# Kernel optimization log

Hardware: AMD Instinct MI355X
Metric: run time of the kernel (lower is better)

Reference implementation:

```python
import math
import jax, jax.numpy as jnp
import numpy as np

# ---- static hyperparams (match init_kwargs) ----
B, D, K, NC, F = 16384, 64, 128, 64, 256
TAU_MIN = 0.01
TAU_DENOM_MIN = 0.001
EPS = 0.001  # transport_eps


def setup_inputs() -> dict:
    key = jax.random.key(0)
    ks = jax.random.split(key, 8)
    # latent positions strictly inside the Poincare ball (norm < 0.9)
    z = jax.random.normal(ks[0], (B, D), jnp.float32)
    z = z / (jnp.linalg.norm(z, axis=-1, keepdims=True) + 1e-6)
    z = z * (0.9 * jax.random.uniform(ks[1], (B, 1), jnp.float32))
    features = jax.random.normal(ks[2], (B, F), jnp.float32)
    q_z_w = jax.random.normal(ks[3], (K, D), jnp.float32) * 0.02
    q_z_b = jnp.zeros((K,), jnp.float32)
    q_feat_w = jax.random.normal(ks[4], (K, F), jnp.float32) * 0.02
    q_feat_b = jnp.zeros((K,), jnp.float32)
    q_gamma = jax.random.normal(ks[5], (K, D, D), jnp.float32) * 0.02
    chart_queries = jax.random.normal(ks[6], (NC, K), jnp.float32) * 0.02
    return {"z": z, "features": features, "q_z_w": q_z_w, "q_z_b": q_z_b,
            "q_feat_w": q_feat_w, "q_feat_b": q_feat_b, "q_gamma": q_gamma,
            "chart_queries": chart_queries}


def _hyperbolic_score(z, centers):
    # z: [B, D]; centers: [NC, D] -> scores [B, NC]
    diff = z[:, None, :] - centers[None, :, :]
    dist_sq = (diff ** 2).sum(-1)                       # [B, NC]
    z_sq = (z ** 2).sum(-1, keepdims=True)              # [B, 1]
    c_sq = (centers ** 2).sum(-1)[None, :]              # [1, NC]
    denom = (1.0 - z_sq) * (1.0 - c_sq)
    arg = 1.0 + 2.0 * dist_sq / (denom + EPS)
    dist = jnp.arccosh(jnp.maximum(arg, 1.0 + EPS))
    # metric-aware temperature tau(z)
    tau = math.sqrt(K) * jnp.maximum(1.0 - z_sq[:, 0], TAU_DENOM_MIN) / 2.0
    tau = jnp.maximum(tau, TAU_MIN)                     # [B]
    return -dist / tau[:, None]


def reference(z, features, q_z_w, q_z_b, q_feat_w, q_feat_b, q_gamma, chart_queries):
    # chart centers live in the first D coords of the chart queries
    centers = chart_queries[:, :D]                      # [NC, D]
    scores = _hyperbolic_score(z, centers)              # [B, NC]

    # query: linear(z) + linear(features) + bilinear gamma term
    q = z @ q_z_w.T + q_z_b + features @ q_feat_w.T + q_feat_b   # [B, K]
    q = q + jnp.einsum("bi,bj,kij->bk", z, z, q_gamma)           # gamma contraction

    # O(n) hyperbolic parallel transport: scale queries by 1/lambda(z)
    r2 = jnp.minimum((z ** 2).sum(-1, keepdims=True), 1.0 - EPS)  # [B, 1]
    lam = 2.0 / (1.0 - r2 + EPS)                                  # [B, 1]
    tq = chart_queries[None, :, :] / lam[:, None, :]              # [B, NC, K]

    scores = scores + jnp.einsum("bk,bnk->bn", q, tq) / math.sqrt(K)
    weights = jax.nn.softmax(scores, axis=-1)           # [B, NC] (soft routing)
    k_chart = jnp.argmax(weights, axis=-1)              # [B]
    return weights, k_chart
```

## Files before the change

kernel.cpp:

```cpp
#include <hip/hip_runtime.h>
#include <hip/hip_bf16.h>
#include <cmath>
#include <cstring>

#define B_TOT 16384

typedef unsigned int uint_t;
typedef unsigned short ushort_t;
typedef __attribute__((ext_vector_type(8))) short bf16x8;
typedef __attribute__((ext_vector_type(16))) float f32x16;

#define WS_TAB 0
#define WS_CSQ 1024
#define WS_LIN 4096
#define WS_S   4198400
#define WS_PPK 5246976

__global__ __launch_bounds__(256) void prep_s(const float* __restrict__ g,
                                              const float* __restrict__ cq,
                                              char* __restrict__ ws) {
  __shared__ float gl[128][68];
  __shared__ float cql[16][132];
  float* S = (float*)(ws + WS_S);
  const int ns = blockIdx.x >> 6, J = blockIdx.x & 63, t = threadIdx.x;
  for (int i = t; i < 2048; i += 256) {
    const int k = i >> 4, c4 = (i & 15) * 4;
    *(float4*)&gl[k][c4] = *(const float4*)(g + (size_t)k * 4096 + J * 64 + c4);
  }
  for (int i = t; i < 2048; i += 256) {
    const int n16 = i >> 7, k = i & 127;
    cql[n16][k] = cq[(ns * 16 + n16) * 128 + k];
  }
  __syncthreads();
  const int n16 = t >> 4, c4 = (t & 15) * 4;
  float4 acc = {0.f, 0.f, 0.f, 0.f};
#pragma unroll 8
  for (int k = 0; k < 128; ++k) {
    const float w = cql[n16][k];
    const float4 gv = *(const float4*)&gl[k][c4];
    acc.x = fmaf(w, gv.x, acc.x);
    acc.y = fmaf(w, gv.y, acc.y);
    acc.z = fmaf(w, gv.z, acc.z);
    acc.w = fmaf(w, gv.w, acc.w);
  }
  *(float4*)(S + (size_t)(ns * 16 + n16) * 4096 + J * 64 + c4) = acc;
}

__global__ __launch_bounds__(256) void prep_pack(
    const float* __restrict__ qfw, const float* __restrict__ cq,
    const float* __restrict__ qzw, const float* __restrict__ qzb,
    const float* __restrict__ qfb, char* __restrict__ ws) {
  __shared__ float Sl[4096];
  __shared__ uint_t tabl[192];
  __shared__ float psumf[128][2];
  const int n = blockIdx.x & 63, part = blockIdx.x >> 6, t = threadIdx.x;
  const float* __restrict__ S = (const float*)(ws + WS_S) + (size_t)n * 4096;
  for (int i = t; i < 4096; i += 256) Sl[i] = S[i];
  if (t < 64) {
    const int i = t;
    const int start = (i < 16) ? 4 * i
                     : (i < 32) ? 64 + 3 * (i - 16)
                     : (i < 48) ? 112 + 2 * (i - 32)
                                : 144 + (i - 48);
    const int nst = 4 - (i >> 4);
    for (int u = 0; u < nst; ++u)
      tabl[start + u] = (0u << 16) | ((uint_t)i << 8) | (uint_t)(16 * ((i >> 4) + u));
  } else if (t < 80) tabl[160 + (t - 64)] = (1u << 16) | (uint_t)((t - 64) * 16);
  else if (t < 84)   tabl[176 + (t - 80)] = (2u << 16) | (uint_t)((t - 80) * 16);
  else if (t == 84)  tabl[180] = (3u << 16);
  else if (t < 96)   tabl[181 + (t - 85)] = 0;
  __syncthreads();
  if (part == 0 && n == 0 && t < 192) ((uint_t*)(ws + WS_TAB))[t] = tabl[t];

  const int mt = n >> 5, r = n & 31;
  auto wpack = [&](int s, int jo, float val) {
    const __hip_bfloat16 hb = __float2bfloat16(val);
    const float hf = __bfloat162float(hb);
    const __hip_bfloat16 lb = __float2bfloat16(val - hf);
    ushort_t hu, lu;
    memcpy(&hu, &hb, 2);
    memcpy(&lu, &lb, 2);
    const size_t base =
        (((size_t)s * 4 + mt * 2) * 64 + ((jo >> 3) & 1) * 32 + r) * 16 + (jo & 7) * 2;
    *(ushort_t*)(ws + WS_PPK + base) = hu;
    *(ushort_t*)(ws + WS_PPK + base + 1024) = lu;
  };

  for (int v = part * 640 + t; v < (part + 1) * 640; v += 256) {
    const int s = v >> 4, jo = v & 15;
    const uint_t inf = tabl[s];
    const int i = (inf >> 8) & 255, j0 = inf & 255;
    const int j = j0 + jo;
    const float val =
        (j < i) ? 0.f : ((j > i) ? Sl[i * 64 + j] + Sl[j * 64 + i] : Sl[i * 64 + i]);
    wpack(s, jo, val);
  }
  const float* __restrict__ cqn = cq + n * 128;

  if (part >= 2) {
    const int fl = t & 127, kh = t >> 7;
    const int f = (part - 2) * 128 + fl;
    float a = 0.f;
#pragma unroll 8
    for (int k = 0; k < 64; ++k)
      a = fmaf(qfw[(kh * 64 + k) * 256 + f], cqn[kh * 64 + k], a);
    psumf[fl][kh] = a;
    __syncthreads();
    if (t < 128) {
      const int ff = (part - 2) * 128 + t;
      wpack(160 + (ff >> 4), ff & 15, psumf[t][0] + psumf[t][1]);
    }
  } else if (part == 1) {
    if (t < 64) {
      float a = 0.f;
#pragma unroll 8
      for (int k = 0; k < 128; ++k) a = fmaf(cqn[k], qzw[k * 64 + t], a);
      wpack(176 + (t >> 4), t & 15, a);
    }
    for (int v2 = t; v2 < 176; v2 += 256) wpack(181 + (v2 >> 4), v2 & 15, 0.f);
  } else {
    if (t == 128) {
      float a = 0.f;
      for (int k = 0; k < 128; ++k) a = fmaf(qzb[k] + qfb[k], cqn[k], a);
      wpack(180, 0, a);
    } else if (t > 128 && t < 144) wpack(180, t - 128, 0.f);
    if (t == 144) {
      double a = 0.0;
      for (int d = 0; d < 64; ++d) a = fma((double)cqn[d], (double)cqn[d], a);
      ((double*)(ws + WS_CSQ))[n] = a;
    }
  }
}

__global__ __launch_bounds__(256, 4) void gemm_tail_kernel(
    const float* __restrict__ z, const float* __restrict__ feat,
    const float* __restrict__ cq, char* __restrict__ ws,
    float* __restrict__ out) {
  __shared__ __align__(16) unsigned char smem[46208];
  float (*z_lds)[68] = (float (*)[68])(smem);
  float (*s_lin)[65] = (float (*)[65])(smem + 8704);
  float (*zt)[33] = (float (*)[33])(smem + 17024);
  float (*cqT)[65] = (float (*)[65])(smem + 25472);
  double (*s_exp)[65] = (double (*)[65])(smem + 25472);
  double (*pmax)[9] = (double (*)[9])(smem + 42112);
  int (*parg)[9] = (int (*)[9])(smem + 44416);
  double* rowmax = (double*)(smem + 45568);
  int* rowarg = (int*)(smem + 45824);
  double* rowinv = (double*)(smem + 45952);

  const int t = threadIdx.x, lane = t & 63;
  const int wv = __builtin_amdgcn_readfirstlane(t >> 6);
  const int b0 = blockIdx.x * 32;
  const int h = lane >> 5, c = lane & 31;

  for (int i = t; i < 2048; i += 256) z_lds[i >> 6][i & 63] = z[(size_t)b0 * 64 + i];
  if (t < 128) z_lds[t >> 2][64 + (t & 3)] = 0.f;
  for (int i = t; i < 32 * 65; i += 256) ((float*)s_lin)[i] = 0.f;
  __syncthreads();

  const bf16x8* __restrict__ pp = (const bf16x8*)(ws + WS_PPK);
  const uint_t* __restrict__ tab = (const uint_t*)(ws + WS_TAB);
  f32x16 acc[2] = {};
#pragma unroll 2
  for (int it = 0; it < 46; ++it) {
    const int s = wv + it * 4;
    const uint_t inf = tab[s];
    const int mode = inf >> 16, i_idx = (inf >> 8) & 255, p0 = inf & 255;
    const bf16x8 Ah0 = pp[((size_t)s * 4 + 0) * 64 + lane];
    const bf16x8 Al0 = pp[((size_t)s * 4 + 1) * 64 + lane];
    const bf16x8 Ah1 = pp[((size_t)s * 4 + 2) * 64 + lane];
    const bf16x8 Al1 = pp[((size_t)s * 4 + 3) * 64 + lane];
    const int bl = c;
    float xv[8];
    if (mode == 0) {
      const float zi = z_lds[bl][i_idx];
      const float* __restrict__ zp = &z_lds[bl][p0 + h * 8];
      const float4 a = *(const float4*)zp, b2 = *(const float4*)(zp + 4);
      xv[0] = zi * a.x; xv[1] = zi * a.y; xv[2] = zi * a.z; xv[3] = zi * a.w;
      xv[4] = zi * b2.x; xv[5] = zi * b2.y; xv[6] = zi * b2.z; xv[7] = zi * b2.w;
    } else if (mode == 1) {
      const float* __restrict__ fp = feat + (size_t)(b0 + bl) * 256 + p0 + h * 8;
      const float4 a = *(const float4*)fp, b2 = *(const float4*)(fp + 4);
      xv[0] = a.x; xv[1] = a.y; xv[2] = a.z; xv[3] = a.w;
      xv[4] = b2.x; xv[5] = b2.y; xv[6] = b2.z; xv[7] = b2.w;
    } else if (mode == 2) {
      const float* __restrict__ zp = &z_lds[bl][p0 + h * 8];
      const float4 a = *(const float4*)zp, b2 = *(const float4*)(zp + 4);
      xv[0] = a.x; xv[1] = a.y; xv[2] = a.z; xv[3] = a.w;
      xv[4] = b2.x; xv[5] = b2.y; xv[6] = b2.z; xv[7] = b2.w;
    } else {
      xv[0] = (h == 0) ? 1.f : 0.f;
      xv[1] = xv[2] = xv[3] = xv[4] = xv[5] = xv[6] = xv[7] = 0.f;
    }
    uint_t bhw[4], blw[4];
#pragma unroll
    for (int e2 = 0; e2 < 4; ++e2) {
      const float2 xp = {xv[2 * e2], xv[2 * e2 + 1]};
      const __hip_bfloat162 hb2 = __float22bfloat162_rn(xp);
      uint_t hw;
      memcpy(&hw, &hb2, 4);
      const float h0 = __uint_as_float(hw << 16);
      const float h1 = __uint_as_float(hw & 0xffff0000u);
      const float2 lp = {xp.x - h0, xp.y - h1};
      const __hip_bfloat162 lb2 = __float22bfloat162_rn(lp);
      uint_t lw;
      memcpy(&lw, &lb2, 4);
      bhw[e2] = hw;
      blw[e2] = lw;
    }
    bf16x8 Bh, Bl;
    memcpy(&Bh, bhw, 16);
    memcpy(&Bl, blw, 16);
    acc[0] = __builtin_amdgcn_mfma_f32_32x32x16_bf16(Ah0, Bh, acc[0], 0, 0, 0);
    acc[0] = __builtin_amdgcn_mfma_f32_32x32x16_bf16(Ah0, Bl, acc[0], 0, 0, 0);
    acc[0] = __builtin_amdgcn_mfma_f32_32x32x16_bf16(Al0, Bh, acc[0], 0, 0, 0);
    acc[1] = __builtin_amdgcn_mfma_f32_32x32x16_bf16(Ah1, Bh, acc[1], 0, 0, 0);
    acc[1] = __builtin_amdgcn_mfma_f32_32x32x16_bf16(Ah1, Bl, acc[1], 0, 0, 0);
    acc[1] = __builtin_amdgcn_mfma_f32_32x32x16_bf16(Al1, Bh, acc[1], 0, 0, 0);
  }
#pragma unroll
  for (int mt = 0; mt < 2; ++mt)
#pragma unroll
    for (int r = 0; r < 16; ++r) {
      const int n = mt * 32 + (r & 3) + 8 * (r >> 2) + 4 * h;
      atomicAdd(&s_lin[c][n], acc[mt][r]);
    }

  for (int i = t; i < 2048; i += 256) zt[i & 63][i >> 6] = z[(size_t)b0 * 64 + i];
  for (int i = t; i < 4096; i += 256) {
    const int n = i >> 6, ii = i & 63;
    cqT[ii][n] = cq[n * 128 + ii];
  }
  __syncthreads();

  const int r = t & 31, cg = t >> 5;

  double z_sq = 0.0, zc[8] = {0.0, 0.0, 0.0, 0.0, 0.0, 0.0, 0.0, 0.0};
#pragma unroll 4
  for (int i = 0; i < 64; ++i) {
    const double zv = (double)zt[i][r];
    z_sq = fma(zv, zv, z_sq);
#pragma unroll
    for (int u = 0; u < 8; ++u)
      zc[u] = fma(zv, (double)cqT[i][cg + 8 * u], zc[u]);
  }
  float lin[8];
#pragma unroll
  for (int u = 0; u < 8; ++u) lin[u] = s_lin[r][cg + 8 * u];

  const double EPS = 0.001;
  const double SQRTK = sqrt(128.0);
  double tau = SQRTK * fmax(1.0 - z_sq, 0.001) * 0.5;
  tau = fmax(tau, 0.01);
  const double inv_tau = 1.0 / tau;
  const double r2 = fmin(z_sq, 1.0 - EPS);
  const double lam_fac = (1.0 - r2 + EPS) * 0.5 / SQRTK;
  const double* __restrict__ csqd = (const double*)(ws + WS_CSQ);

  double sc[8];
#pragma unroll
  for (int u = 0; u < 8; ++u) {
    const int n = cg + 8 * u;
    const double c_sq = csqd[n];
    const double dist_sq = z_sq + c_sq - 2.0 * zc[u];
    const double denom = (1.0 - z_sq) * (1.0 - c_sq);
    float df = 2.0f * (float)dist_sq / ((float)denom + 0.001f);
    df = fmaxf(df, 0.001f);
    const float root = sqrtf(df * (df + 2.0f));
    const float dist = log1pf(df + root);
    sc[u] = -(double)dist * inv_tau + (double)lin[u] * lam_fac;
  }
  __syncthreads();

  {
    double mx = sc[0];
    int am = cg;
#pragma unroll
    for (int u = 1; u < 8; ++u)
      if (sc[u] > mx) { mx = sc[u]; am = cg + 8 * u; }
    pmax[r][cg] = mx;
    parg[r][cg] = am;
  }
  __syncthreads();
  if (t < 32) {
    double m = pmax[t][0];
    int a = parg[t][0];
#pragma unroll
    for (int g = 1; g < 8; ++g) {
      const double v = pmax[t][g];
      const int aa = parg[t][g];
      if (v > m || (v == m && aa < a)) { m = v; a = aa; }
    }
    rowmax[t] = m;
    rowarg[t] = a;
  }
  __syncthreads();
  {
    const double m = rowmax[r];
    double ps = 0.0;
#pragma unroll
    for (int u = 0; u < 8; ++u) {
      const double e = (double)expf((float)(sc[u] - m));
      s_exp[r][cg + 8 * u] = e;
      ps += e;
    }
    pmax[r][cg] = ps;
  }
  __syncthreads();
  if (t < 32) {
    double s = 0.0;
#pragma unroll
    for (int g = 0; g < 8; ++g) s += pmax[t][g];
    rowinv[t] = 1.0 / s;
  }
  __syncthreads();
  for (int idx = t; idx < 2048; idx += 256) {
    const int b = idx >> 6, n = idx & 63;
    out[(size_t)(b0 + b) * 64 + n] = (float)(s_exp[b][n] * rowinv[b]);
  }
  if (t < 32) out[(size_t)B_TOT * 64 + b0 + t] = (float)rowarg[t];
}

extern "C" void kernel_launch(void* const* d_in, const int* in_sizes, int n_in,
                              void* d_out, int out_size, void* d_ws, size_t ws_size,
                              hipStream_t stream) {
  const float* z = (const float*)d_in[0];
  const float* feat = (const float*)d_in[1];
  const float* qzw = (const float*)d_in[2];
  const float* qzb = (const float*)d_in[3];
  const float* qfw = (const float*)d_in[4];
  const float* qfb = (const float*)d_in[5];
  const float* gamma = (const float*)d_in[6];
  const float* cq = (const float*)d_in[7];
  float* out = (float*)d_out;
  char* ws = (char*)d_ws;

  prep_s<<<dim3(256), dim3(256), 0, stream>>>(gamma, cq, ws);
  prep_pack<<<dim3(256), dim3(256), 0, stream>>>(qfw, cq, qzw, qzb, qfb, ws);
  gemm_tail_kernel<<<dim3(B_TOT / 32), dim3(256), 0, stream>>>(z, feat, cq, ws, out);
}
```

Baseline: 154.1 us.

## Specialize GEMM loop phases, prefetch features, replace LDS atomics with per-wave reduction

The table-driven loop, which branched per step on a mode word loaded from workspace, is split into specialized phases. Index math for the z-outer-product steps is computed inline, the feature rows are prefetched into registers before the first barrier, and the linear and bias steps run as separate tail calls. LDS atomicAdd accumulation of the MFMA results is replaced by per-wave partial slabs followed by a barrier and a 4-way sum. This removes divergent branching, table loads and atomic contention, at the cost of more registers for the prefetched features, an extra barrier, and a hard-coded step layout that must match the packing kernel.

New measurement: 141.3 us. -8.3%, faster.

```diff
diff --git a/kernel.cpp b/kernel.cpp
--- a/kernel.cpp
+++ b/kernel.cpp
@@ -138,7 +138,7 @@
     float* __restrict__ out) {
   __shared__ __align__(16) unsigned char smem[46208];
   float (*z_lds)[68] = (float (*)[68])(smem);
-  float (*s_lin)[65] = (float (*)[65])(smem + 8704);
+  float (*slin)[65] = (float (*)[65])(smem + 8704);
   float (*zt)[33] = (float (*)[33])(smem + 17024);
   float (*cqT)[65] = (float (*)[65])(smem + 25472);
   double (*s_exp)[65] = (double (*)[65])(smem + 25472);
@@ -153,45 +153,27 @@
   const int b0 = blockIdx.x * 32;
   const int h = lane >> 5, c = lane & 31;
 
+  float4 fva[4], fvb[4];
+#pragma unroll
+  for (int m = 0; m < 4; ++m) {
+    const float* __restrict__ fp =
+        feat + (size_t)(b0 + c) * 256 + (4 * m + wv) * 16 + h * 8;
+    fva[m] = *(const float4*)fp;
+    fvb[m] = *(const float4*)(fp + 4);
+  }
+
   for (int i = t; i < 2048; i += 256) z_lds[i >> 6][i & 63] = z[(size_t)b0 * 64 + i];
   if (t < 128) z_lds[t >> 2][64 + (t & 3)] = 0.f;
-  for (int i = t; i < 32 * 65; i += 256) ((float*)s_lin)[i] = 0.f;
   __syncthreads();
 
   const bf16x8* __restrict__ pp = (const bf16x8*)(ws + WS_PPK);
-  const uint_t* __restrict__ tab = (const uint_t*)(ws + WS_TAB);
   f32x16 acc[2] = {};
-#pragma unroll 2
-  for (int it = 0; it < 46; ++it) {
-    const int s = wv + it * 4;
-    const uint_t inf = tab[s];
-    const int mode = inf >> 16, i_idx = (inf >> 8) & 255, p0 = inf & 255;
+
+  auto do_mfma = [&](const float* xv, int s) {
     const bf16x8 Ah0 = pp[((size_t)s * 4 + 0) * 64 + lane];
     const bf16x8 Al0 = pp[((size_t)s * 4 + 1) * 64 + lane];
     const bf16x8 Ah1 = pp[((size_t)s * 4 + 2) * 64 + lane];
     const bf16x8 Al1 = pp[((size_t)s * 4 + 3) * 64 + lane];
-    const int bl = c;
-    float xv[8];
-    if (mode == 0) {
-      const float zi = z_lds[bl][i_idx];
-      const float* __restrict__ zp = &z_lds[bl][p0 + h * 8];
-      const float4 a = *(const float4*)zp, b2 = *(const float4*)(zp + 4);
-      xv[0] = zi * a.x; xv[1] = zi * a.y; xv[2] = zi * a.z; xv[3] = zi * a.w;
-      xv[4] = zi * b2.x; xv[5] = zi * b2.y; xv[6] = zi * b2.z; xv[7] = zi * b2.w;
-    } else if (mode == 1) {
-      const float* __restrict__ fp = feat + (size_t)(b0 + bl) * 256 + p0 + h * 8;
-      const float4 a = *(const float4*)fp, b2 = *(const float4*)(fp + 4);
-      xv[0] = a.x; xv[1] = a.y; xv[2] = a.z; xv[3] = a.w;
-      xv[4] = b2.x; xv[5] = b2.y; xv[6] = b2.z; xv[7] = b2.w;
-    } else if (mode == 2) {
-      const float* __restrict__ zp = &z_lds[bl][p0 + h * 8];
-      const float4 a = *(const float4*)zp, b2 = *(const float4*)(zp + 4);
-      xv[0] = a.x; xv[1] = a.y; xv[2] = a.z; xv[3] = a.w;
-      xv[4] = b2.x; xv[5] = b2.y; xv[6] = b2.z; xv[7] = b2.w;
-    } else {
-      xv[0] = (h == 0) ? 1.f : 0.f;
-      xv[1] = xv[2] = xv[3] = xv[4] = xv[5] = xv[6] = xv[7] = 0.f;
-    }
     uint_t bhw[4], blw[4];
 #pragma unroll
     for (int e2 = 0; e2 < 4; ++e2) {
@@ -217,14 +199,64 @@
     acc[1] = __builtin_amdgcn_mfma_f32_32x32x16_bf16(Ah1, Bh, acc[1], 0, 0, 0);
     acc[1] = __builtin_amdgcn_mfma_f32_32x32x16_bf16(Ah1, Bl, acc[1], 0, 0, 0);
     acc[1] = __builtin_amdgcn_mfma_f32_32x32x16_bf16(Al1, Bh, acc[1], 0, 0, 0);
-  }
-#pragma unroll
-  for (int mt = 0; mt < 2; ++mt)
-#pragma unroll
-    for (int r = 0; r < 16; ++r) {
-      const int n = mt * 32 + (r & 3) + 8 * (r >> 2) + 4 * h;
-      atomicAdd(&s_lin[c][n], acc[mt][r]);
-    }
+  };
+
+#pragma unroll 2
+  for (int it = 0; it < 40; ++it) {
+    const int s = wv + it * 4;
+    int i_idx, p0;
+    if (s < 64) {
+      i_idx = s >> 2; p0 = (s & 3) * 16;
+    } else if (s < 112) {
+      const int q = s - 64, d = (q * 86) >> 8;
+      i_idx = 16 + d; p0 = (q - 3 * d + 1) * 16;
+    } else if (s < 144) {
+      const int q = s - 112;
+      i_idx = 32 + (q >> 1); p0 = ((q & 1) + 2) * 16;
+    } else {
+      i_idx = s - 96; p0 = 48;
+    }
+    const float zi = z_lds[c][i_idx];
+    const float* __restrict__ zp = &z_lds[c][p0 + h * 8];
+    const float4 a = *(const float4*)zp, b2 = *(const float4*)(zp + 4);
+    const float xv[8] = {zi * a.x, zi * a.y, zi * a.z, zi * a.w,
+                         zi * b2.x, zi * b2.y, zi * b2.z, zi * b2.w};
+    do_mfma(xv, s);
+  }
+#pragma unroll
+  for (int m = 0; m < 4; ++m) {
+    const float xv[8] = {fva[m].x, fva[m].y, fva[m].z, fva[m].w,
+                         fvb[m].x, fvb[m].y, fvb[m].z, fvb[m].w};
+    do_mfma(xv, 160 + 4 * m + wv);
+  }
+  {
+    const float* __restrict__ zp = &z_lds[c][wv * 16 + h * 8];
+    const float4 a = *(const float4*)zp, b2 = *(const float4*)(zp + 4);
+    const float xv[8] = {a.x, a.y, a.z, a.w, b2.x, b2.y, b2.z, b2.w};
+    do_mfma(xv, 176 + wv);
+  }
+  {
+    const float xv[8] = {(h == 0) ? 1.f : 0.f, 0.f, 0.f, 0.f, 0.f, 0.f, 0.f, 0.f};
+    do_mfma(xv, 180 + wv);
+  }
+
+  {
+    float* __restrict__ slw = (float*)(smem + 8704) + wv * 2080;
+#pragma unroll
+    for (int mt = 0; mt < 2; ++mt)
+#pragma unroll
+      for (int r = 0; r < 16; ++r) {
+        const int n = mt * 32 + (r & 3) + 8 * (r >> 2) + 4 * h;
+        slw[c * 65 + n] = acc[mt][r];
+      }
+  }
+  __syncthreads();
+  for (int idx = t; idx < 2048; idx += 256) {
+    const int c0 = idx >> 6, n0 = idx & 63;
+    float* __restrict__ base = (float*)(smem + 8704) + c0 * 65 + n0;
+    base[0] = (base[0] + base[2080]) + (base[4160] + base[6240]);
+  }
+  __syncthreads();
 
   for (int i = t; i < 2048; i += 256) zt[i & 63][i >> 6] = z[(size_t)b0 * 64 + i];
   for (int i = t; i < 4096; i += 256) {
@@ -246,7 +278,7 @@
   }
   float lin[8];
 #pragma unroll
-  for (int u = 0; u < 8; ++u) lin[u] = s_lin[r][cg + 8 * u];
+  for (int u = 0; u < 8; ++u) lin[u] = slin[r][cg + 8 * u];
 
   const double EPS = 0.001;
   const double SQRTK = sqrt(128.0);
```
